# Performance work log

Measured on AMD Instinct MI355X. Metric: run time of the kernel, lower is better.

## Reference

```python
import jax, jax.numpy as jnp
import numpy as np

B, N = 2, 256
IN_N = 32          # input node features
H = 8              # per-layer default num_heads (GAT does not override it)
HN, HE = 64, 64    # hidden node / edge features per head
DN, DE = HN * H, HE * H  # 512, 512
OUT_N = 32


def _gat_layer(nodes, edges, mask, Wn, bn, We, be, Wa):
    # nodes: [b,n,dn_in], edges: [b,n,n,de_in], mask: [b,n] bool
    nf = nodes @ Wn + bn                                   # [b,n,DN]
    ef = jnp.einsum('bije,ef->bijf', edges, We) + be       # [b,n,n,DE]
    q = nf @ Wa                                            # [b,n,H]
    qe = jnp.einsum('bijf,fh->bijh', ef, Wa)               # [b,n,n,H]
    sn = jnp.einsum('bik,bjk->bij', q, q) / np.float32(np.sqrt(HN))
    se = jnp.einsum('bik,bijk->bij', q, qe) / np.float32(np.sqrt(HE))
    m = mask[..., None]
    wn = jax.nn.softmax(sn * m, axis=-1)                   # [b,n,n]
    we = jax.nn.softmax(se * m, axis=-1)                   # [b,n,n]
    awn = jnp.einsum('bij,bik->bjk', wn, nf)               # [b,n,DN]
    agg_e = jnp.einsum('bij,bijk->bik', we, ef)            # [b,n,DE]
    upd_nodes = nf + awn + agg_e                           # [b,n,DN]
    upd_edges = ef + we[..., None] * ef + jnp.einsum('bij,bik->bijk', wn, nf)
    re = jax.nn.elu(upd_edges)                             # [b,n,n,DE]
    re = (re + jnp.swapaxes(re, 1, 2)) / 2
    return jax.nn.elu(upd_nodes), re


def setup_inputs() -> dict:
    key = jax.random.key(0)
    ks = jax.random.split(key, 16)
    s = 0.05
    return {
        'nodes': jax.random.normal(ks[0], (B, N, IN_N), jnp.float32),
        'edges': jax.random.normal(ks[1], (B, N, N), jnp.float32),
        'node_mask': jnp.ones((B, N), dtype=bool),
        # layer 1 params
        'Wn1': jax.random.normal(ks[2], (IN_N, DN), jnp.float32) * s,
        'bn1': jnp.zeros((DN,), jnp.float32),
        'We1': jax.random.normal(ks[3], (1, DE), jnp.float32) * s,
        'be1': jnp.zeros((DE,), jnp.float32),
        'Wa1': jax.random.normal(ks[4], (DN, H), jnp.float32) * s,
        # layer 2 params
        'Wn2': jax.random.normal(ks[5], (DN, DN), jnp.float32) * s,
        'bn2': jnp.zeros((DN,), jnp.float32),
        'We2': jax.random.normal(ks[6], (DE, DE), jnp.float32) * s,
        'be2': jnp.zeros((DE,), jnp.float32),
        'Wa2': jax.random.normal(ks[7], (DN, H), jnp.float32) * s,
        # final projections
        'Wfn': jax.random.normal(ks[8], (DN, OUT_N), jnp.float32) * s,
        'bfn': jnp.zeros((OUT_N,), jnp.float32),
        'Wfe': jax.random.normal(ks[9], (DE, 1), jnp.float32) * s,
        'bfe': jnp.zeros((1,), jnp.float32),
    }


def reference(nodes, edges, node_mask, Wn1, bn1, We1, be1, Wa1,
              Wn2, bn2, We2, be2, Wa2, Wfn, bfn, Wfe, bfe):
    e = edges[..., None]                      # [b,n,n,1]
    e = (e + jnp.swapaxes(e, 1, 2)) / 2       # symmetrize
    e = jax.nn.relu(e)
    n, e = _gat_layer(nodes, e, node_mask, Wn1, bn1, We1, be1, Wa1)
    n, e = _gat_layer(n, e, node_mask, Wn2, bn2, We2, be2, Wa2)
    out_nodes = jnp.tanh(n @ Wfn + bfn)                                   # [b,n,OUT_N]
    out_edges = jnp.tanh(jnp.einsum('bijf,fo->bijo', e, Wfe) + bfe)[..., 0]  # [b,n,n]
    return out_nodes, out_edges
```

## Files before the change

### kernel.cpp

```cpp
#include <hip/hip_runtime.h>
#include <hip/hip_bf16.h>
#include <stdint.h>


typedef __attribute__((ext_vector_type(8))) short short8v;
typedef __attribute__((ext_vector_type(4))) float f32x4;

__device__ __forceinline__ float eluf(float x) { return x > 0.f ? x : (__expf(x) - 1.f); }

__device__ __forceinline__ short f2bf(float x) {
  union { float f; unsigned u; } v; v.f = x;
  unsigned r = v.u + 0x7fffu + ((v.u >> 16) & 1u);
  return (short)(r >> 16);
}
__device__ __forceinline__ float bf2f(short s) {
  union { unsigned u; float f; } v; v.u = ((unsigned)(unsigned short)s) << 16; return v.f;
}

template<int OP>
__device__ float blockRed256(float v, float* s4) {
#pragma unroll
  for (int o = 32; o; o >>= 1) { float t = __shfl_xor(v, o); v = OP ? fmaxf(v, t) : v + t; }
  int w = threadIdx.x >> 6;
  __syncthreads();
  if ((threadIdx.x & 63) == 0) s4[w] = v;
  __syncthreads();
  return OP ? fmaxf(fmaxf(s4[0], s4[1]), fmaxf(s4[2], s4[3]))
            : (s4[0] + s4[1] + s4[2] + s4[3]);
}

__global__ __launch_bounds__(256) void k01(const float* __restrict__ We2,
    const float* __restrict__ Wa2, const float* __restrict__ We1,
    const float* __restrict__ be1, const float* __restrict__ be2,
    const float* __restrict__ Wa1, const float* __restrict__ nodes,
    const float* __restrict__ Wn1, const float* __restrict__ bn1,
    short* __restrict__ Bp, float* __restrict__ M2,
    float* __restrict__ u1, float* __restrict__ v1, float* __restrict__ vb2,
    short* __restrict__ Wb1b, float* __restrict__ nf1, short* __restrict__ nf1b,
    float* __restrict__ q1) {
  int bid = blockIdx.x;
  if (bid >= 258) {
    __shared__ float nrow[32];
    __shared__ float qL[8];
    int bi = bid - 258; int tid = threadIdx.x;
    if (tid < 32) nrow[tid] = nodes[bi * 32 + tid];
    if (tid < 8) qL[tid] = 0.f;
    __syncthreads();
    int f0 = tid, f1 = tid + 256;
    float a0 = bn1[f0], a1 = bn1[f1];
#pragma unroll 8
    for (int c = 0; c < 32; c++) {
      float nv = nrow[c];
      a0 += nv * Wn1[c * 512 + f0];
      a1 += nv * Wn1[c * 512 + f1];
    }
    nf1[(size_t)bi * 512 + f0] = a0;
    nf1[(size_t)bi * 512 + f1] = a1;
    nf1b[(size_t)bi * 512 + f0] = f2bf(a0);
    nf1b[(size_t)bi * 512 + f1] = f2bf(a1);
    const float* wa0 = Wa1 + f0 * 8;
    const float* wa1 = Wa1 + f1 * 8;
#pragma unroll
    for (int h = 0; h < 8; h++) {
      float v = a0 * wa0[h] + a1 * wa1[h];
      for (int o = 32; o; o >>= 1) v += __shfl_xor(v, o);
      if ((tid & 63) == 0) atomicAdd(&qL[h], v);
    }
    __syncthreads();
    if (tid < 8) q1[bi * 8 + tid] = qL[tid];
    return;
  }
  if (bid < 128) {
    int id = bid * 256 + threadIdx.x;
    int c = id >> 11; int rem = id & 2047; int g = rem >> 9; int n = rem & 511;
    short8v v;
#pragma unroll
    for (int e = 0; e < 8; e++) v[e] = f2bf(We2[(c * 32 + g * 8 + e) * 512 + n]);
    int pos = n * 4 + (g ^ ((n >> 1) & 3));
    *(short8v*)(Bp + (c * 2048 + pos) * 8) = v;
    return;
  }
  if (bid == 257) {
    for (int idx = threadIdx.x; idx < 1024; idx += 256) {
      int g = idx >> 4, e = idx & 15;
      Wb1b[idx] = f2bf(e < 8 ? We1[g * 8 + e] : be1[g * 8 + (e - 8)]);
    }
    return;
  }
  int lane = threadIdx.x & 63;
  int idx = (bid - 128) * 4 + (threadIdx.x >> 6);
  if (idx < 512) {
    float a[8] = {0, 0, 0, 0, 0, 0, 0, 0};
    for (int k0 = lane; k0 < 512; k0 += 64) {
      float wv = We2[idx * 512 + k0];
      const float* wa = Wa2 + k0 * 8;
#pragma unroll
      for (int h = 0; h < 8; h++) a[h] += wv * wa[h];
    }
#pragma unroll
    for (int h = 0; h < 8; h++) {
      float v = a[h];
      for (int o = 32; o; o >>= 1) v += __shfl_xor(v, o);
      if (lane == 0) M2[idx * 8 + h] = v;
    }
  } else if (idx < 515) {
    const float* src = (idx == 512) ? We1 : (idx == 513 ? be1 : be2);
    const float* Wa = (idx == 514) ? Wa2 : Wa1;
    float* dst = (idx == 512) ? u1 : (idx == 513 ? v1 : vb2);
    float a[8] = {0, 0, 0, 0, 0, 0, 0, 0};
    for (int f = lane; f < 512; f += 64) {
      float s = src[f];
#pragma unroll
      for (int h = 0; h < 8; h++) a[h] += s * Wa[f * 8 + h];
    }
#pragma unroll
    for (int h = 0; h < 8; h++) {
      float v = a[h];
      for (int o = 32; o; o >>= 1) v += __shfl_xor(v, o);
      if (lane == 0) dst[h] = v;
    }
  }
}

__global__ __launch_bounds__(256) void k2_l1attn(const float* __restrict__ edges,
    const float* __restrict__ q1, const float* __restrict__ u1, const float* __restrict__ v1,
    float* __restrict__ e0, float* __restrict__ wn1, float* __restrict__ we1,
    float* __restrict__ tt) {
  __shared__ float s4[4];
  int bi = blockIdx.x; int b = bi >> 8; int i = bi & 255; int j = threadIdx.x;
  float qi[8], qj[8];
#pragma unroll
  for (int h = 0; h < 8; h++) { qi[h] = q1[bi * 8 + h]; qj[h] = q1[(b * 256 + j) * 8 + h]; }
  float eij = edges[bi * 256 + j];
  float eji = edges[(b * 256 + j) * 256 + i];
  float e0v = fmaxf(0.f, 0.5f * (eij + eji));
  e0[bi * 256 + j] = e0v;
  float sn = 0.f, aI = 0.f, cI = 0.f;
#pragma unroll
  for (int h = 0; h < 8; h++) { sn += qi[h] * qj[h]; aI += qi[h] * u1[h]; cI += qi[h] * v1[h]; }
  sn *= 0.125f;
  float se = (aI * e0v + cI) * 0.125f;
  float mn = blockRed256<1>(sn, s4);
  float en = __expf(sn - mn);
  float sumn = blockRed256<0>(en, s4);
  float wnv = en / sumn; wn1[bi * 256 + j] = wnv;
  float me = blockRed256<1>(se, s4);
  float ee = __expf(se - me);
  float sume = blockRed256<0>(ee, s4);
  float wev = ee / sume; we1[bi * 256 + j] = wev;
  float t = blockRed256<0>(wev * e0v, s4);
  if (j == 0) tt[bi] = t;
}

__global__ __launch_bounds__(512) void k34(const float* __restrict__ nf1,
    const float* __restrict__ wn1, const float* __restrict__ tt,
    const float* __restrict__ We1, const float* __restrict__ be1,
    const float* __restrict__ Wn2, const float* __restrict__ bn2,
    const float* __restrict__ Wa2, const float* __restrict__ M2,
    const float* __restrict__ vb2, float* __restrict__ nf2, float* __restrict__ q2,
    float* __restrict__ p2, float* __restrict__ cst) {
  __shared__ float n1L[2][512];
  __shared__ float qL[2][8];
  int bx = blockIdx.x;
  int b = bx >> 7; int x0 = (bx & 127) * 2; int k = threadIdx.x;
  int g0 = b * 256 + x0;
  float a0 = 0.f, a1 = 0.f;
#pragma unroll 4
  for (int i = 0; i < 256; i++) {
    float nv = nf1[(size_t)(b * 256 + i) * 512 + k];
    a0 += wn1[(b * 256 + i) * 256 + x0] * nv;
    a1 += wn1[(b * 256 + i) * 256 + x0 + 1] * nv;
  }
  float w = We1[k], be = be1[k];
  n1L[0][k] = eluf(nf1[(size_t)g0 * 512 + k] + a0 + tt[g0] * w + be);
  n1L[1][k] = eluf(nf1[(size_t)(g0 + 1) * 512 + k] + a1 + tt[g0 + 1] * w + be);
  if (k < 16) qL[k >> 3][k & 7] = 0.f;
  __syncthreads();
  float acc0 = bn2[k], acc1 = bn2[k];
#pragma unroll 4
  for (int g = 0; g < 512; g++) {
    float wv = Wn2[g * 512 + k];
    acc0 += n1L[0][g] * wv; acc1 += n1L[1][g] * wv;
  }
  nf2[(size_t)g0 * 512 + k] = acc0;
  nf2[(size_t)(g0 + 1) * 512 + k] = acc1;
  const float* wa = Wa2 + k * 8;
#pragma unroll
  for (int h = 0; h < 8; h++) {
    float v0 = acc0 * wa[h], v1 = acc1 * wa[h];
    for (int o = 32; o; o >>= 1) { v0 += __shfl_xor(v0, o); v1 += __shfl_xor(v1, o); }
    if ((k & 63) == 0) { atomicAdd(&qL[0][h], v0); atomicAdd(&qL[1][h], v1); }
  }
  __syncthreads();
  float q0[8], q1v[8];
#pragma unroll
  for (int h = 0; h < 8; h++) { q0[h] = qL[0][h]; q1v[h] = qL[1][h]; }
  if (k < 8) { q2[g0 * 8 + k] = q0[k]; q2[(g0 + 1) * 8 + k] = q1v[k]; }
  float p0 = 0.f, p1 = 0.f; const float* m2 = M2 + k * 8;
#pragma unroll
  for (int h = 0; h < 8; h++) { p0 += m2[h] * q0[h]; p1 += m2[h] * q1v[h]; }
  p2[(size_t)g0 * 512 + k] = p0;
  p2[(size_t)(g0 + 1) * 512 + k] = p1;
  if (k == 0) {
    float c0 = 0.f, c1 = 0.f;
#pragma unroll
    for (int h = 0; h < 8; h++) { c0 += q0[h] * vb2[h]; c1 += q1v[h] * vb2[h]; }
    cst[g0] = c0; cst[g0 + 1] = c1;
  }
}

__global__ __launch_bounds__(256) void k5b_pairs(const float* __restrict__ nf1,
    const float* __restrict__ p2, const float* __restrict__ e0,
    const float* __restrict__ wn1, const float* __restrict__ we1,
    const float* __restrict__ We1, const float* __restrict__ be1,
    const float* __restrict__ cst, float* __restrict__ se2) {
  __shared__ float NI[16 * 132], NJ[16 * 132], PI[16 * 132], PJ[16 * 132];
  __shared__ float W1[128], B1[128];
  int bid = blockIdx.x; int b = bid & 1; int pr = bid >> 1;
  int I = 0;
  { int p = pr; while (p >= 16 - I) { p -= 16 - I; I++; } pr = p; }
  int J = I + pr;
  int I0 = I * 16, J0 = J * 16;
  int tid = threadIdx.x; int ii = tid & 15, jj = tid >> 4;
  int gi = b * 256 + I0 + ii, gj = b * 256 + J0 + jj;
  int ij = gi * 256 + (J0 + jj), ji = gj * 256 + (I0 + ii);
  float e0v = e0[ij];
  float s1 = 1.f + we1[ij], w1 = wn1[ij];
  float s2 = 1.f + we1[ji], w2 = wn1[ji];
  float dot1 = 0.f, dot2 = 0.f;
  for (int fc = 0; fc < 4; fc++) {
    __syncthreads();
    int f00 = fc * 128;
    for (int t = tid; t < 2048; t += 256) {
      int row = t >> 7, f = t & 127;
      NI[row * 132 + f] = nf1[(size_t)(b * 256 + I0 + row) * 512 + f00 + f];
      NJ[row * 132 + f] = nf1[(size_t)(b * 256 + J0 + row) * 512 + f00 + f];
      PI[row * 132 + f] = p2[(size_t)(b * 256 + I0 + row) * 512 + f00 + f];
      PJ[row * 132 + f] = p2[(size_t)(b * 256 + J0 + row) * 512 + f00 + f];
    }
    if (tid < 128) { W1[tid] = We1[f00 + tid]; B1[tid] = be1[f00 + tid]; }
    __syncthreads();
#pragma unroll 8
    for (int f = 0; f < 128; f += 4) {
      float4 niv = *(const float4*)&NI[ii * 132 + f];
      float4 njv = *(const float4*)&NJ[jj * 132 + f];
      float4 piv = *(const float4*)&PI[ii * 132 + f];
      float4 pjv = *(const float4*)&PJ[jj * 132 + f];
      float4 wv = *(const float4*)&W1[f];
      float4 bv = *(const float4*)&B1[f];
      float ni_[4] = {niv.x, niv.y, niv.z, niv.w};
      float nj_[4] = {njv.x, njv.y, njv.z, njv.w};
      float pi_[4] = {piv.x, piv.y, piv.z, piv.w};
      float pj_[4] = {pjv.x, pjv.y, pjv.z, pjv.w};
      float w_[4] = {wv.x, wv.y, wv.z, wv.w};
      float b_[4] = {bv.x, bv.y, bv.z, bv.w};
#pragma unroll
      for (int e = 0; e < 4; e++) {
        float ef = e0v * w_[e] + b_[e];
        float x1 = ef * s1 + w1 * ni_[e];
        float x2 = ef * s2 + w2 * nj_[e];
        float e1v = 0.5f * (eluf(x1) + eluf(x2));
        dot1 += e1v * pi_[e];
        dot2 += e1v * pj_[e];
      }
    }
  }
  se2[ij] = (dot1 + cst[gi]) * 0.125f;
  se2[ji] = (dot2 + cst[gj]) * 0.125f;
}

__global__ __launch_bounds__(256) void k5ackz(const float* __restrict__ q2,
    const float* __restrict__ se2, const float* __restrict__ nf1,
    const float* __restrict__ e0, const float* __restrict__ wn1,
    const float* __restrict__ we1, const float* __restrict__ We1,
    const float* __restrict__ be1, float* __restrict__ wn2, float* __restrict__ we2,
    float* __restrict__ Z) {
  __shared__ float s4[4];
  __shared__ float e0L[256], s1L[256], w1L[256], s2L[256], w2L[256], weL[256];
  int bi = blockIdx.x; int b = bi >> 8; int i = bi & 255; int j = threadIdx.x;
  float sn = 0.f;
#pragma unroll
  for (int h = 0; h < 8; h++) sn += q2[bi * 8 + h] * q2[(b * 256 + j) * 8 + h];
  sn *= 0.125f;
  float mn = blockRed256<1>(sn, s4);
  float en = __expf(sn - mn);
  float s = blockRed256<0>(en, s4);
  wn2[bi * 256 + j] = en / s;
  float se = se2[bi * 256 + j];
  float me = blockRed256<1>(se, s4);
  float ee = __expf(se - me);
  float s2s = blockRed256<0>(ee, s4);
  float wev = ee / s2s;
  we2[bi * 256 + j] = wev;
  e0L[j] = e0[bi * 256 + j];
  s1L[j] = 1.f + we1[bi * 256 + j];
  w1L[j] = wn1[bi * 256 + j];
  weL[j] = wev;
  s2L[j] = 1.f + we1[(b * 256 + j) * 256 + i];
  w2L[j] = wn1[(b * 256 + j) * 256 + i];
  __syncthreads();
  int k0 = j, k1 = j + 256;
  float W0 = We1[k0], B0 = be1[k0], W1 = We1[k1], B1 = be1[k1];
  float ni0 = nf1[(size_t)bi * 512 + k0], ni1 = nf1[(size_t)bi * 512 + k1];
  float z0 = 0.f, z1 = 0.f;
  const float* nfb = nf1 + (size_t)b * 256 * 512;
#pragma unroll 2
  for (int jj = 0; jj < 256; jj++) {
    float e0v = e0L[jj], s1 = s1L[jj], w1 = w1L[jj], s2 = s2L[jj], w2 = w2L[jj], we = weL[jj];
    const float* nj = nfb + (size_t)jj * 512;
    float nj0 = nj[k0], nj1 = nj[k1];
    float ef0 = e0v * W0 + B0;
    float x10 = ef0 * s1 + w1 * ni0, x20 = ef0 * s2 + w2 * nj0;
    z0 += we * 0.5f * (eluf(x10) + eluf(x20));
    float ef1 = e0v * W1 + B1;
    float x11 = ef1 * s1 + w1 * ni1, x21 = ef1 * s2 + w2 * nj1;
    z1 += we * 0.5f * (eluf(x11) + eluf(x21));
  }
  Z[(size_t)bi * 512 + k0] = z0;
  Z[(size_t)bi * 512 + k1] = z1;
}

__global__ __launch_bounds__(256, 2) void k6_main(
    const short* __restrict__ nf1b, const float* __restrict__ nf2,
    const float* __restrict__ e0, const float* __restrict__ wn1, const float* __restrict__ we1,
    const float* __restrict__ wn2, const float* __restrict__ we2,
    const float* __restrict__ be2, const float* __restrict__ Wfe,
    const float* __restrict__ bfe, const short* __restrict__ Bp,
    const short* __restrict__ Wb1b, float* __restrict__ Dout, float* __restrict__ oute) {
  __shared__ __align__(16) short As[2][2048];
  __shared__ __align__(16) short nfIb[16 * 512];
  __shared__ __align__(16) short nfJb[4 * 512];
  __shared__ __align__(16) short WbL[1024];
  __shared__ float e0r[64], s1r[64], w1r[64], s2r[64], w2r[64];
  __shared__ float weAr[64], wnAr[64], weBr[64], wnBr[64];
  __shared__ float dsumA[64], dsumB[64];

  int bid = (blockIdx.x & 7) * 136 + (blockIdx.x >> 3);
  int b = bid & 1; int rest = bid >> 1;
  int Jq = rest & 3; int pr = rest >> 2;
  int I = 0;
  { int p = pr; while (p >= 16 - I) { p -= 16 - I; I++; } pr = p; }
  int J = I + pr;
  int I0 = I * 16, J0 = J * 16 + Jq * 4;
  bool dual = (I != J);

  int tid = threadIdx.x, lane = tid & 63, w = tid >> 6;
  int g4 = lane >> 4;

  for (int t = tid; t < 1024; t += 256) {
    int row = t >> 6, g = t & 63;
    *(short8v*)(nfIb + row * 512 + g * 8) =
        *(const short8v*)(nf1b + (size_t)(b * 256 + I0 + row) * 512 + g * 8);
  }
  {
    int row = tid >> 6, g = tid & 63;
    *(short8v*)(nfJb + row * 512 + g * 8) =
        *(const short8v*)(nf1b + (size_t)(b * 256 + J0 + row) * 512 + g * 8);
  }
  if (tid < 128) *(short8v*)(WbL + tid * 8) = *(const short8v*)(Wb1b + tid * 8);
  if (tid < 64) {
    int i = I0 + (tid & 15), j = J0 + (tid >> 4);
    int ij = (b * 256 + i) * 256 + j, ji = (b * 256 + j) * 256 + i;
    e0r[tid] = e0[ij];
    s1r[tid] = 1.f + we1[ij]; w1r[tid] = wn1[ij];
    s2r[tid] = 1.f + we1[ji]; w2r[tid] = wn1[ji];
    weAr[tid] = we2[ij]; wnAr[tid] = wn2[ij];
    weBr[tid] = we2[ji]; wnBr[tid] = wn2[ji];
    dsumA[tid] = 0.f; dsumB[tid] = 0.f;
  }
  __syncthreads();

  int ar = tid >> 2;
  int ac = tid & 3;
  const short* niB = nfIb + (ar & 15) * 512;
  const short* njB = nfJb + (ar >> 4) * 512;
  float e0v = e0r[ar], s1 = s1r[ar], w1 = w1r[ar], s2 = s2r[ar], w2 = w2r[ar];
  int apos8 = (ar * 4 + (ac ^ ((ar >> 1) & 3))) * 8;

  auto genA = [&](int cg, short* dst) {
    int gI = cg * 4 + ac;
    short8v niq = *(const short8v*)(niB + gI * 8);
    short8v njq = *(const short8v*)(njB + gI * 8);
    short8v wq = *(const short8v*)(WbL + gI * 16);
    short8v bq = *(const short8v*)(WbL + gI * 16 + 8);
    short8v pk;
#pragma unroll
    for (int e = 0; e < 8; e++) {
      float ef = e0v * bf2f(wq[e]) + bf2f(bq[e]);
      float x1 = ef * s1 + w1 * bf2f(niq[e]);
      float x2 = ef * s2 + w2 * bf2f(njq[e]);
      float v = 0.5f * (eluf(x1) + eluf(x2));
      pk[e] = f2bf(v);
    }
    *(short8v*)(dst + apos8) = pk;
  };

  int boff[8];
#pragma unroll
  for (int nf = 0; nf < 8; nf++) {
    int n = w * 128 + nf * 16 + (lane & 15);
    boff[nf] = (n * 4 + (g4 ^ ((n >> 1) & 3))) * 8;
  }

  float be2v[8], wfev[8];
#pragma unroll
  for (int nf = 0; nf < 8; nf++) {
    int k = w * 128 + nf * 16 + (lane & 15);
    be2v[nf] = be2[k]; wfev[nf] = Wfe[k];
  }
  f32x4 acc[4][8];
#pragma unroll
  for (int mi = 0; mi < 4; mi++)
#pragma unroll
    for (int nf = 0; nf < 8; nf++)
      acc[mi][nf] = (f32x4){be2v[nf], be2v[nf], be2v[nf], be2v[nf]};

  genA(0, As[0]);
  __syncthreads();

  for (int c = 0; c < 16; ++c) {
    int cur = c & 1;
    const short* bbase = Bp + c * 16384;
    short8v bf[8];
#pragma unroll
    for (int nf = 0; nf < 8; nf++) bf[nf] = *(const short8v*)(bbase + boff[nf]);
    if (c < 15) genA(c + 1, As[cur ^ 1]);
    short8v a[4];
#pragma unroll
    for (int mi = 0; mi < 4; mi++) {
      int row = mi * 16 + (lane & 15);
      int cpos = row * 4 + (g4 ^ ((row >> 1) & 3));
      a[mi] = *(const short8v*)(As[cur] + cpos * 8);
    }
#pragma unroll
    for (int nf = 0; nf < 8; nf++)
#pragma unroll
      for (int mi = 0; mi < 4; mi++)
        acc[mi][nf] = __builtin_amdgcn_mfma_f32_16x16x32_bf16(a[mi], bf[nf], acc[mi][nf], 0, 0, 0);
    __syncthreads();
  }

#pragma unroll
  for (int mi = 0; mi < 4; mi++) {
    int jRow = J0 + mi;
    const float* nf2j = nf2 + (size_t)(b * 256 + jRow) * 512;
#pragma unroll
    for (int r4 = 0; r4 < 4; r4++) {
      int jl = mi * 16 + g4 * 4 + r4;
      int iRow = I0 + g4 * 4 + r4;
      const float* nf2i = nf2 + (size_t)(b * 256 + iRow) * 512;
      float sEA = 1.f + weAr[jl], wNA = wnAr[jl];
      float sEB = 1.f + weBr[jl], wNB = wnBr[jl];
      float dvA = 0.f, dvB = 0.f;
#pragma unroll
      for (int nf = 0; nf < 8; nf++) {
        int k = w * 128 + nf * 16 + (lane & 15);
        float ef2 = acc[mi][nf][r4];
        float UA = ef2 * sEA + wNA * nf2i[k];
        dvA += eluf(UA) * wfev[nf];
        if (dual) {
          float UB = ef2 * sEB + wNB * nf2j[k];
          dvB += eluf(UB) * wfev[nf];
        }
      }
#pragma unroll
      for (int o = 1; o < 16; o <<= 1) dvA += __shfl_xor(dvA, o);
      if ((lane & 15) == 0) atomicAdd(&dsumA[jl], dvA);
      if (dual) {
#pragma unroll
        for (int o = 1; o < 16; o <<= 1) dvB += __shfl_xor(dvB, o);
        if ((lane & 15) == 0) atomicAdd(&dsumB[jl], dvB);
      }
    }
  }
  __syncthreads();
  if (tid < 64) {
    int i = I0 + (tid & 15), j = J0 + (tid >> 4);
    if (dual) {
      float v = tanhf(0.5f * (dsumA[tid] + dsumB[tid]) + bfe[0]);
      oute[(size_t)(b * 256 + i) * 256 + j] = v;
      oute[(size_t)(b * 256 + j) * 256 + i] = v;
    } else {
      Dout[(size_t)(b * 256 + i) * 256 + j] = dsumA[tid];
    }
  }
}

__global__ __launch_bounds__(512) void k78(const float* __restrict__ nf2,
    const float* __restrict__ wn2, const float* __restrict__ Z,
    const float* __restrict__ We2, const float* __restrict__ be2,
    const float* __restrict__ Wfn, const float* __restrict__ bfn,
    const float* __restrict__ Dm, const float* __restrict__ bfe,
    float* __restrict__ outn, float* __restrict__ oute) {
  int bx = blockIdx.x; int k = threadIdx.x;
  if (bx >= 256) {
    if (k < 256) {
      int d = bx - 256; int b = d >> 4; int I0 = (d & 15) * 16;
      int r = k >> 4, c = k & 15;
      int gi = b * 256 + I0 + r, gj = b * 256 + I0 + c;
      float v = 0.5f * (Dm[(size_t)gi * 256 + I0 + c] + Dm[(size_t)gj * 256 + I0 + r]) +
                bfe[0];
      oute[(size_t)gi * 256 + I0 + c] = tanhf(v);
    }
    return;
  }
  __shared__ float zL[2][512];
  __shared__ float n2L[2][512];
  __shared__ float red[512];
  int b = bx >> 7; int x0 = (bx & 127) * 2;
  int g0 = b * 256 + x0;
  zL[0][k] = Z[(size_t)g0 * 512 + k];
  zL[1][k] = Z[(size_t)(g0 + 1) * 512 + k];
  float a0 = 0.f, a1 = 0.f;
#pragma unroll 4
  for (int i = 0; i < 256; i++) {
    float nv = nf2[(size_t)(b * 256 + i) * 512 + k];
    a0 += wn2[(b * 256 + i) * 256 + x0] * nv;
    a1 += wn2[(b * 256 + i) * 256 + x0 + 1] * nv;
  }
  __syncthreads();
  float ag0 = be2[k], ag1 = be2[k];
#pragma unroll 4
  for (int g = 0; g < 512; g++) {
    float wv = We2[g * 512 + k];
    ag0 += zL[0][g] * wv; ag1 += zL[1][g] * wv;
  }
  n2L[0][k] = eluf(nf2[(size_t)g0 * 512 + k] + a0 + ag0);
  n2L[1][k] = eluf(nf2[(size_t)(g0 + 1) * 512 + k] + a1 + ag1);
  __syncthreads();
  int row = k >> 8, t = k & 255;
  int o = t & 31, part = t >> 5;
  float acc = 0.f;
  for (int f = part * 64; f < part * 64 + 64; f++) acc += n2L[row][f] * Wfn[f * 32 + o];
  red[k] = acc;
  __syncthreads();
  if (k < 64) {
    int r2 = k >> 5, o2 = k & 31;
    float s = 0.f;
#pragma unroll
    for (int p = 0; p < 8; p++) s += red[r2 * 256 + p * 32 + o2];
    outn[(size_t)(g0 + r2) * 32 + o2] = tanhf(s + bfn[o2]);
  }
}

extern "C" void kernel_launch(void* const* d_in, const int* in_sizes, int n_in,
                              void* d_out, int out_size, void* d_ws, size_t ws_size,
                              hipStream_t stream) {
  const float* nodes = (const float*)d_in[0];
  const float* edges = (const float*)d_in[1];
  const float* Wn1 = (const float*)d_in[3];
  const float* bn1 = (const float*)d_in[4];
  const float* We1 = (const float*)d_in[5];
  const float* be1 = (const float*)d_in[6];
  const float* Wa1 = (const float*)d_in[7];
  const float* Wn2 = (const float*)d_in[8];
  const float* bn2 = (const float*)d_in[9];
  const float* We2 = (const float*)d_in[10];
  const float* be2 = (const float*)d_in[11];
  const float* Wa2 = (const float*)d_in[12];
  const float* Wfn = (const float*)d_in[13];
  const float* bfn = (const float*)d_in[14];
  const float* Wfe = (const float*)d_in[15];
  const float* bfe = (const float*)d_in[16];

  float* ws = (float*)d_ws;
  size_t off = 0;
  float* nf1 = ws + off; off += 262144;
  float* q1 = ws + off; off += 4096;
  float* e0 = ws + off; off += 131072;
  float* wn1 = ws + off; off += 131072;
  float* we1 = ws + off; off += 131072;
  float* tt = ws + off; off += 512;
  float* nf2 = ws + off; off += 262144;
  float* q2 = ws + off; off += 4096;
  float* p2 = ws + off; off += 262144;
  float* cst = ws + off; off += 512;
  float* wn2 = ws + off; off += 131072;
  float* we2 = ws + off; off += 131072;
  float* M2 = ws + off; off += 4096;
  float* u1 = ws + off; off += 8;
  float* v1 = ws + off; off += 8;
  float* vb2 = ws + off; off += 16;
  float* se2 = ws + off; off += 131072;
  float* Zb = ws + off; off += 262144;
  float* Dm = ws + off; off += 131072;
  short* nf1b = (short*)(ws + off); off += 131072;
  short* Bp = (short*)(ws + off); off += 131072;
  short* Wb1b = (short*)(ws + off); off += 512;

  float* outn = (float*)d_out;
  float* oute = outn + 2 * 256 * 32;

  hipLaunchKernelGGL(k01, dim3(770), dim3(256), 0, stream, We2, Wa2, We1, be1, be2, Wa1,
                     nodes, Wn1, bn1, Bp, M2, u1, v1, vb2, Wb1b, nf1, nf1b, q1);
  hipLaunchKernelGGL(k2_l1attn, dim3(512), dim3(256), 0, stream, edges, q1, u1, v1, e0, wn1,
                     we1, tt);
  hipLaunchKernelGGL(k34, dim3(256), dim3(512), 0, stream, nf1, wn1, tt, We1, be1,
                     Wn2, bn2, Wa2, M2, vb2, nf2, q2, p2, cst);
  hipLaunchKernelGGL(k5b_pairs, dim3(272), dim3(256), 0, stream, nf1, p2, e0, wn1, we1, We1,
                     be1, cst, se2);
  hipLaunchKernelGGL(k5ackz, dim3(512), dim3(256), 0, stream, q2, se2, nf1, e0, wn1, we1,
                     We1, be1, wn2, we2, Zb);
  hipLaunchKernelGGL(k6_main, dim3(1088), dim3(256), 0, stream, nf1b, nf2, e0, wn1, we1,
                     wn2, we2, be2, Wfe, bfe, Bp, Wb1b, Dm, oute);
  hipLaunchKernelGGL(k78, dim3(288), dim3(512), 0, stream, nf2, wn2, Zb, We2, be2, Wfn, bfn,
                     Dm, bfe, outn, oute);
}
```

Baseline: 341.5 us.

## Generate MFMA A-operands in registers per wave instead of via shared buffer

The k6_main GEMM no longer builds the A tile cooperatively into a double-buffered shared-memory array. Each wave now computes its own A fragments directly in registers in MFMA operand layout, which removes the shared A buffer, its writes and reads, and the per-chunk __syncthreads. In exchange every wave redundantly recomputes the full A elementwise transform (ELU, bf16 packing), roughly 4x more VALU work, and the nf row stride is padded to 520 to avoid LDS bank conflicts. Separately, an earlier reduction loop is unrolled by 4 instead of 2.

```diff
diff --git a/kernel.cpp b/kernel.cpp
--- a/kernel.cpp
+++ b/kernel.cpp
@@ -304,7 +304,7 @@
   float ni0 = nf1[(size_t)bi * 512 + k0], ni1 = nf1[(size_t)bi * 512 + k1];
   float z0 = 0.f, z1 = 0.f;
   const float* nfb = nf1 + (size_t)b * 256 * 512;
-#pragma unroll 2
+#pragma unroll 4
   for (int jj = 0; jj < 256; jj++) {
     float e0v = e0L[jj], s1 = s1L[jj], w1 = w1L[jj], s2 = s2L[jj], w2 = w2L[jj], we = weL[jj];
     const float* nj = nfb + (size_t)jj * 512;
@@ -327,9 +327,8 @@
     const float* __restrict__ be2, const float* __restrict__ Wfe,
     const float* __restrict__ bfe, const short* __restrict__ Bp,
     const short* __restrict__ Wb1b, float* __restrict__ Dout, float* __restrict__ oute) {
-  __shared__ __align__(16) short As[2][2048];
-  __shared__ __align__(16) short nfIb[16 * 512];
-  __shared__ __align__(16) short nfJb[4 * 512];
+  __shared__ __align__(16) short nfIb[16 * 520];
+  __shared__ __align__(16) short nfJb[4 * 520];
   __shared__ __align__(16) short WbL[1024];
   __shared__ float e0r[64], s1r[64], w1r[64], s2r[64], w2r[64];
   __shared__ float weAr[64], wnAr[64], weBr[64], wnBr[64];
@@ -346,15 +345,16 @@
 
   int tid = threadIdx.x, lane = tid & 63, w = tid >> 6;
   int g4 = lane >> 4;
+  int n15 = lane & 15;
 
   for (int t = tid; t < 1024; t += 256) {
     int row = t >> 6, g = t & 63;
-    *(short8v*)(nfIb + row * 512 + g * 8) =
+    *(short8v*)(nfIb + row * 520 + g * 8) =
         *(const short8v*)(nf1b + (size_t)(b * 256 + I0 + row) * 512 + g * 8);
   }
   {
     int row = tid >> 6, g = tid & 63;
-    *(short8v*)(nfJb + row * 512 + g * 8) =
+    *(short8v*)(nfJb + row * 520 + g * 8) =
         *(const short8v*)(nf1b + (size_t)(b * 256 + J0 + row) * 512 + g * 8);
   }
   if (tid < 128) *(short8v*)(WbL + tid * 8) = *(const short8v*)(Wb1b + tid * 8);
@@ -370,76 +370,62 @@
   }
   __syncthreads();
 
-  int ar = tid >> 2;
-  int ac = tid & 3;
-  const short* niB = nfIb + (ar & 15) * 512;
-  const short* njB = nfJb + (ar >> 4) * 512;
-  float e0v = e0r[ar], s1 = s1r[ar], w1 = w1r[ar], s2 = s2r[ar], w2 = w2r[ar];
-  int apos8 = (ar * 4 + (ac ^ ((ar >> 1) & 3))) * 8;
-
-  auto genA = [&](int cg, short* dst) {
-    int gI = cg * 4 + ac;
+  float e0v[4], s1v[4], w1v[4], s2v[4], w2v[4];
+#pragma unroll
+  for (int jj = 0; jj < 4; jj++) {
+    int r = jj * 16 + n15;
+    e0v[jj] = e0r[r]; s1v[jj] = s1r[r]; w1v[jj] = w1r[r];
+    s2v[jj] = s2r[r]; w2v[jj] = w2r[r];
+  }
+  const short* niB = nfIb + n15 * 520;
+
+  int boff[8];
+#pragma unroll
+  for (int nf = 0; nf < 8; nf++) {
+    int n = w * 128 + nf * 16 + n15;
+    boff[nf] = (n * 4 + (g4 ^ ((n >> 1) & 3))) * 8;
+  }
+
+  f32x4 acc[4][8];
+  {
+#pragma unroll
+    for (int nf = 0; nf < 8; nf++) {
+      float bv = be2[w * 128 + nf * 16 + n15];
+#pragma unroll
+      for (int mi = 0; mi < 4; mi++) acc[mi][nf] = (f32x4){bv, bv, bv, bv};
+    }
+  }
+
+  for (int c = 0; c < 16; ++c) {
+    const short* bbase = Bp + c * 16384;
+    short8v bfv[8];
+#pragma unroll
+    for (int nf = 0; nf < 8; nf++) bfv[nf] = *(const short8v*)(bbase + boff[nf]);
+    int gI = c * 4 + g4;
     short8v niq = *(const short8v*)(niB + gI * 8);
-    short8v njq = *(const short8v*)(njB + gI * 8);
     short8v wq = *(const short8v*)(WbL + gI * 16);
     short8v bq = *(const short8v*)(WbL + gI * 16 + 8);
-    short8v pk;
-#pragma unroll
-    for (int e = 0; e < 8; e++) {
-      float ef = e0v * bf2f(wq[e]) + bf2f(bq[e]);
-      float x1 = ef * s1 + w1 * bf2f(niq[e]);
-      float x2 = ef * s2 + w2 * bf2f(njq[e]);
-      float v = 0.5f * (eluf(x1) + eluf(x2));
-      pk[e] = f2bf(v);
-    }
-    *(short8v*)(dst + apos8) = pk;
-  };
-
-  int boff[8];
-#pragma unroll
-  for (int nf = 0; nf < 8; nf++) {
-    int n = w * 128 + nf * 16 + (lane & 15);
-    boff[nf] = (n * 4 + (g4 ^ ((n >> 1) & 3))) * 8;
-  }
-
-  float be2v[8], wfev[8];
-#pragma unroll
-  for (int nf = 0; nf < 8; nf++) {
-    int k = w * 128 + nf * 16 + (lane & 15);
-    be2v[nf] = be2[k]; wfev[nf] = Wfe[k];
-  }
-  f32x4 acc[4][8];
-#pragma unroll
-  for (int mi = 0; mi < 4; mi++)
-#pragma unroll
-    for (int nf = 0; nf < 8; nf++)
-      acc[mi][nf] = (f32x4){be2v[nf], be2v[nf], be2v[nf], be2v[nf]};
-
-  genA(0, As[0]);
-  __syncthreads();
-
-  for (int c = 0; c < 16; ++c) {
-    int cur = c & 1;
-    const short* bbase = Bp + c * 16384;
-    short8v bf[8];
-#pragma unroll
-    for (int nf = 0; nf < 8; nf++) bf[nf] = *(const short8v*)(bbase + boff[nf]);
-    if (c < 15) genA(c + 1, As[cur ^ 1]);
-    short8v a[4];
-#pragma unroll
-    for (int mi = 0; mi < 4; mi++) {
-      int row = mi * 16 + (lane & 15);
-      int cpos = row * 4 + (g4 ^ ((row >> 1) & 3));
-      a[mi] = *(const short8v*)(As[cur] + cpos * 8);
-    }
-#pragma unroll
-    for (int nf = 0; nf < 8; nf++)
-#pragma unroll
-      for (int mi = 0; mi < 4; mi++)
-        acc[mi][nf] = __builtin_amdgcn_mfma_f32_16x16x32_bf16(a[mi], bf[nf], acc[mi][nf], 0, 0, 0);
-    __syncthreads();
-  }
-
+#pragma unroll
+    for (int jj = 0; jj < 4; jj++) {
+      short8v njq = *(const short8v*)(nfJb + jj * 520 + gI * 8);
+      short8v aj;
+#pragma unroll
+      for (int e = 0; e < 8; e++) {
+        float ef = e0v[jj] * bf2f(wq[e]) + bf2f(bq[e]);
+        float x1 = ef * s1v[jj] + w1v[jj] * bf2f(niq[e]);
+        float x2 = ef * s2v[jj] + w2v[jj] * bf2f(njq[e]);
+        float v = 0.5f * (eluf(x1) + eluf(x2));
+        aj[e] = f2bf(v);
+      }
+#pragma unroll
+      for (int nf = 0; nf < 8; nf++)
+        acc[jj][nf] = __builtin_amdgcn_mfma_f32_16x16x32_bf16(aj, bfv[nf], acc[jj][nf], 0, 0, 0);
+    }
+  }
+
+  float wfev[8];
+#pragma unroll
+  for (int nf = 0; nf < 8; nf++) wfev[nf] = Wfe[w * 128 + nf * 16 + n15];
 #pragma unroll
   for (int mi = 0; mi < 4; mi++) {
     int jRow = J0 + mi;
@@ -454,7 +440,7 @@
       float dvA = 0.f, dvB = 0.f;
 #pragma unroll
       for (int nf = 0; nf < 8; nf++) {
-        int k = w * 128 + nf * 16 + (lane & 15);
+        int k = w * 128 + nf * 16 + n15;
         float ef2 = acc[mi][nf][r4];
         float UA = ef2 * sEA + wNA * nf2i[k];
         dvA += eluf(UA) * wfev[nf];
```

New measurement: 384.7 us. 1.13x slower.
